# Kernel tuning notes

Measured on AMD Instinct MI355X. Metric: run time of the kernel, lower is better.

## Reference

```python
import jax, jax.numpy as jnp
import numpy as np

NTOKEN = 150000   # len(ui2idx)
NINP   = 64       # opt.d_word_vec
NHID   = 2 * NINP # gnn1 output dim
NEDGE  = 2400000  # hetero static graph edges
B, L   = 64, 200  # batch_size, max_len


def setup_inputs() -> dict:
    key = jax.random.key(0)
    ks = jax.random.split(key, 8)
    def xavier(k, shape):
        scale = (2.0 / (shape[0] + shape[1])) ** 0.5
        return scale * jax.random.normal(k, shape, jnp.float32)
    emb = xavier(ks[0], (NTOKEN, NINP)).at[0].set(0.0)  # padding_idx=0
    W1 = xavier(ks[1], (NINP, NHID))
    b1 = jnp.zeros((NHID,), jnp.float32)
    W2 = xavier(ks[2], (NHID, NINP))
    b2 = jnp.zeros((NINP,), jnp.float32)
    edge_index = jax.random.randint(ks[3], (2, NEDGE), 0, NTOKEN, dtype=jnp.int32).astype(jnp.int64)
    inp = jax.random.randint(ks[4], (B, L), 0, NTOKEN, dtype=jnp.int32).astype(jnp.int64)
    input_timestamp = jax.random.randint(ks[5], (B, L), 0, 300000, dtype=jnp.int32).astype(jnp.int64)
    return {"emb": emb, "W1": W1, "b1": b1, "W2": W2, "b2": b2,
            "input": inp, "input_timestamp": input_timestamp, "edge_index": edge_index}


def gcn_conv(x, W, b, src, dst, n):
    # torch_geometric GCNConv: out = D^{-1/2}(A+I)D^{-1/2} (x W) + b
    h = x @ W                                   # [n, out]
    deg = jnp.zeros((n,), h.dtype).at[dst].add(1.0) + 1.0  # +1 self-loop
    dinv = jax.lax.rsqrt(deg)
    norm = dinv[src] * dinv[dst]                # [E]
    agg = jax.ops.segment_sum(h[src] * norm[:, None], dst, num_segments=n)
    return agg + h * (dinv * dinv)[:, None] + b  # self-loop term + bias


def reference(emb, W1, b1, W2, b2, input, input_timestamp, edge_index):
    src, dst = edge_index[0], edge_index[1]
    h = gcn_conv(emb, W1, b1, src, dst, NTOKEN)      # dropout is identity in eval
    nodes = gcn_conv(h, W2, b2, src, dst, NTOKEN)    # [NTOKEN, NINP]
    # one-hot scatter + einsum 'bt,td->bd' == direct gather
    b_, l_ = input.shape
    return nodes[input.reshape(-1)].reshape(b_, l_, NINP)
```

## Files before the change

### kernel.cpp

```cpp
#include <hip/hip_runtime.h>
#include <hip/hip_bf16.h>

#define NTOKEN 150000
#define NINP   64
#define NEDGE  2400000
#define NPOS   (64*200)

#define NPB    256
#define NBUCK  586
#define EPB    8192
#define NBLK   293
#define CAP    6144

#define O_Z1       0
#define O_HIST     0
#define O_XBF      4800000
#define O_CTOT     9600000
#define O_BSTART   9600640
#define O_DINV     9601280
#define O_ROWSTART 9751296
#define O_BUCK     9901312
#define O_M        12301312
#define O_CVEC     12305408

__device__ __forceinline__ unsigned f2bf(float f) {
    unsigned u = __float_as_uint(f);
    return (u + 0x7FFFu + ((u >> 16) & 1u)) >> 16;
}

__global__ void kX(const float4* __restrict__ X4, uint4* __restrict__ Xbf) {
    int i = blockIdx.x * 256 + threadIdx.x;
    if (i >= NTOKEN * 64 / 8) return;
    float4 a = X4[2 * i], b = X4[2 * i + 1];
    uint4 o;
    o.x = f2bf(a.x) | (f2bf(a.y) << 16);
    o.y = f2bf(a.z) | (f2bf(a.w) << 16);
    o.z = f2bf(b.x) | (f2bf(b.y) << 16);
    o.w = f2bf(b.z) | (f2bf(b.w) << 16);
    Xbf[i] = o;
}

__global__ void kA_hist(const int4* __restrict__ dst4, int* __restrict__ histG) {
    __shared__ int h[NBUCK];
    int tid = threadIdx.x;
    for (int i = tid; i < NBUCK; i += 1024) h[i] = 0;
    __syncthreads();
    int base4 = blockIdx.x * (EPB / 4);
    #pragma unroll
    for (int i = 0; i < EPB / 4096; i++) {
        int idx = base4 + i * 1024 + tid;
        if (idx < NEDGE / 4) {
            int4 d = dst4[idx];
            atomicAdd(&h[d.x >> 8], 1);
            atomicAdd(&h[d.y >> 8], 1);
            atomicAdd(&h[d.z >> 8], 1);
            atomicAdd(&h[d.w >> 8], 1);
        }
    }
    __syncthreads();
    for (int i = tid; i < NBUCK; i += 1024) histG[blockIdx.x * NBUCK + i] = h[i];
}

__global__ void kB1_colscan(int* __restrict__ histG, int* __restrict__ colTotal) {
    __shared__ int sd[256];
    int t = threadIdx.x, b = blockIdx.x;
    int i0 = 2 * t, i1 = 2 * t + 1;
    int v0 = (i0 < NBLK) ? histG[i0 * NBUCK + b] : 0;
    int v1 = (i1 < NBLK) ? histG[i1 * NBUCK + b] : 0;
    int tsum = v0 + v1;
    sd[t] = tsum;
    __syncthreads();
    for (int off = 1; off < 256; off <<= 1) {
        int x = (t >= off) ? sd[t - off] : 0;
        __syncthreads();
        sd[t] += x;
        __syncthreads();
    }
    int excl = sd[t] - tsum;
    if (i0 < NBLK) histG[i0 * NBUCK + b] = excl;
    if (i1 < NBLK) histG[i1 * NBUCK + b] = excl + v0;
    if (t == 255) colTotal[b] = sd[255];
}

__global__ void kB2s(const int* __restrict__ colTotal, int* __restrict__ bucketStart,
                     const float* __restrict__ W1, const float* __restrict__ b1,
                     const float* __restrict__ W2,
                     float* __restrict__ M, float* __restrict__ cvec) {
    int bb = blockIdx.x;
    int t = threadIdx.x;
    if (bb == 0) {
        __shared__ int sd[256];
        int i0 = t * 3, i1 = t * 3 + 1, i2 = t * 3 + 2;
        int v0 = (i0 < NBUCK) ? colTotal[i0] : 0;
        int v1 = (i1 < NBUCK) ? colTotal[i1] : 0;
        int v2 = (i2 < NBUCK) ? colTotal[i2] : 0;
        int tsum = v0 + v1 + v2;
        sd[t] = tsum;
        __syncthreads();
        for (int off = 1; off < 256; off <<= 1) {
            int x = (t >= off) ? sd[t - off] : 0;
            __syncthreads();
            sd[t] += x;
            __syncthreads();
        }
        int excl = sd[t] - tsum;
        if (i0 < NBUCK) bucketStart[i0] = excl;
        if (i1 < NBUCK) bucketStart[i1] = excl + v0;
        if (i2 < NBUCK) bucketStart[i2] = excl + v0 + v1;
        if (t == 255) bucketStart[NBUCK] = NEDGE;
    } else if (bb <= 16) {
        int o = (bb - 1) * 256 + t;
        int i = o >> 6, j = o & 63;
        float s = 0.f;
        #pragma unroll 4
        for (int k = 0; k < 128; k++) s = fmaf(W1[i * 128 + k], W2[k * 64 + j], s);
        M[o] = s;
    } else if (t < 64) {
        float s = 0.f;
        #pragma unroll 4
        for (int k = 0; k < 128; k++) s = fmaf(b1[k], W2[k * 64 + t], s);
        cvec[t] = s;
    }
}

__global__ void kC_scatter(const int4* __restrict__ src4, const int4* __restrict__ dst4,
                           const int* __restrict__ histG, const int* __restrict__ bucketStart,
                           int* __restrict__ bucketPacked) {
    __shared__ int cur[NBUCK];
    int tid = threadIdx.x;
    for (int i = tid; i < NBUCK; i += 1024)
        cur[i] = histG[blockIdx.x * NBUCK + i] + bucketStart[i];
    __syncthreads();
    int base4 = blockIdx.x * (EPB / 4);
    #pragma unroll
    for (int i = 0; i < EPB / 4096; i++) {
        int idx = base4 + i * 1024 + tid;
        if (idx < NEDGE / 4) {
            int4 s = src4[idx];
            int4 d = dst4[idx];
            int p0 = atomicAdd(&cur[d.x >> 8], 1);
            bucketPacked[p0] = (s.x << 8) | (d.x & 255);
            int p1 = atomicAdd(&cur[d.y >> 8], 1);
            bucketPacked[p1] = (s.y << 8) | (d.y & 255);
            int p2 = atomicAdd(&cur[d.z >> 8], 1);
            bucketPacked[p2] = (s.z << 8) | (d.z & 255);
            int p3 = atomicAdd(&cur[d.w >> 8], 1);
            bucketPacked[p3] = (s.w << 8) | (d.w & 255);
        }
    }
}

__global__ void kDE(const int* __restrict__ bucketStart,
                    int* __restrict__ bucketPacked ,
                    float* __restrict__ dinv, int* __restrict__ rowStart) {
    __shared__ int raw[CAP];
    __shared__ int srt[CAP];
    __shared__ int cnt[NPB];
    __shared__ int sd[NPB];
    int t = threadIdx.x, b = blockIdx.x;
    int e0 = bucketStart[b], e1 = bucketStart[b + 1];
    int nE = e1 - e0;
    int nEc = (nE < CAP) ? nE : CAP;
    if (t < NPB) cnt[t] = 0;
    __syncthreads();
    for (int i = t; i < nEc; i += 1024) {
        int p = bucketPacked[e0 + i];
        raw[i] = p;
        atomicAdd(&cnt[p & 255], 1);
    }
    __syncthreads();
    int c = 0;
    if (t < NPB) { c = cnt[t]; sd[t] = c; }
    __syncthreads();
    for (int off = 1; off < 256; off <<= 1) {
        int x = 0;
        if (t < NPB && t >= off) x = sd[t - off];
        __syncthreads();
        if (t < NPB) sd[t] += x;
        __syncthreads();
    }
    if (t < NPB) {
        int excl = sd[t] - c;
        cnt[t] = excl;
        int node = b * NPB + t;
        if (node < NTOKEN) {
            dinv[node] = rsqrtf((float)c + 1.0f);
            rowStart[node] = e0 + excl;
        }
        if (b == NBUCK - 1 && t == 0) rowStart[NTOKEN] = NEDGE;
    }
    __syncthreads();
    for (int i = t; i < nEc; i += 1024) {
        int p = raw[i];
        int pos = atomicAdd(&cnt[p & 255], 1);
        if (pos < CAP) srt[pos] = p >> 8;
    }
    __syncthreads();
    for (int i = t; i < nEc; i += 1024) bucketPacked[e0 + i] = srt[i];
}

__global__ void k_agg(const uint2* __restrict__ Xb, const float* __restrict__ dinv,
                      const int* __restrict__ rowStart, const int* __restrict__ sortedSrc,
                      uint2* __restrict__ Z1b) {
    int g = threadIdx.x >> 4;
    int fl = threadIdx.x & 15;
    int v = blockIdx.x * 16 + g;
    int e0 = rowStart[v], e1 = rowStart[v + 1];
    float dv = dinv[v];
    uint2 xsw = Xb[(size_t)v * 16 + fl];
    float a0x=0.f,a0y=0.f,a0z=0.f,a0w=0.f, a1x=0.f,a1y=0.f,a1z=0.f,a1w=0.f;
    float a2x=0.f,a2y=0.f,a2z=0.f,a2w=0.f, a3x=0.f,a3y=0.f,a3z=0.f,a3w=0.f;
    for (int e = e0; e < e1; e += 8) {
        int m1=e+1<e1, m2=e+2<e1, m3=e+3<e1, m4=e+4<e1, m5=e+5<e1, m6=e+6<e1, m7=e+7<e1;
        int u0 = sortedSrc[e];
        int u1 = sortedSrc[m1 ? e+1 : e];
        int u2 = sortedSrc[m2 ? e+2 : e];
        int u3 = sortedSrc[m3 ? e+3 : e];
        int u4 = sortedSrc[m4 ? e+4 : e];
        int u5 = sortedSrc[m5 ? e+5 : e];
        int u6 = sortedSrc[m6 ? e+6 : e];
        int u7 = sortedSrc[m7 ? e+7 : e];
        float d0 = dinv[u0];
        float d1 = m1 ? dinv[u1] : 0.f;
        float d2 = m2 ? dinv[u2] : 0.f;
        float d3 = m3 ? dinv[u3] : 0.f;
        float d4 = m4 ? dinv[u4] : 0.f;
        float d5 = m5 ? dinv[u5] : 0.f;
        float d6 = m6 ? dinv[u6] : 0.f;
        float d7 = m7 ? dinv[u7] : 0.f;
        uint2 w0 = Xb[(size_t)u0 * 16 + fl];
        uint2 w1 = Xb[(size_t)u1 * 16 + fl];
        uint2 w2 = Xb[(size_t)u2 * 16 + fl];
        uint2 w3 = Xb[(size_t)u3 * 16 + fl];
        uint2 w4 = Xb[(size_t)u4 * 16 + fl];
        uint2 w5 = Xb[(size_t)u5 * 16 + fl];
        uint2 w6 = Xb[(size_t)u6 * 16 + fl];
        uint2 w7 = Xb[(size_t)u7 * 16 + fl];
        #define ACC(d,w,AX,AY,AZ,AW) \
            AX = fmaf(d, __uint_as_float((w).x << 16), AX); \
            AY = fmaf(d, __uint_as_float((w).x & 0xFFFF0000u), AY); \
            AZ = fmaf(d, __uint_as_float((w).y << 16), AZ); \
            AW = fmaf(d, __uint_as_float((w).y & 0xFFFF0000u), AW);
        ACC(d0,w0,a0x,a0y,a0z,a0w)
        ACC(d1,w1,a1x,a1y,a1z,a1w)
        ACC(d2,w2,a2x,a2y,a2z,a2w)
        ACC(d3,w3,a3x,a3y,a3z,a3w)
        ACC(d4,w4,a0x,a0y,a0z,a0w)
        ACC(d5,w5,a1x,a1y,a1z,a1w)
        ACC(d6,w6,a2x,a2y,a2z,a2w)
        ACC(d7,w7,a3x,a3y,a3z,a3w)
        #undef ACC
    }
    float ax = (a0x + a1x) + (a2x + a3x);
    float ay = (a0y + a1y) + (a2y + a3y);
    float az = (a0z + a1z) + (a2z + a3z);
    float aw = (a0w + a1w) + (a2w + a3w);
    float c = dv * dv;
    float ox = c * fmaf(dv, __uint_as_float(xsw.x << 16),        ax);
    float oy = c * fmaf(dv, __uint_as_float(xsw.x & 0xFFFF0000u), ay);
    float oz = c * fmaf(dv, __uint_as_float(xsw.y << 16),        az);
    float ow = c * fmaf(dv, __uint_as_float(xsw.y & 0xFFFF0000u), aw);
    uint2 o;
    o.x = f2bf(ox) | (f2bf(oy) << 16);
    o.y = f2bf(oz) | (f2bf(ow) << 16);
    Z1b[(size_t)v * 16 + fl] = o;
}

__global__ void k_out(const int* __restrict__ inp, const uint2* __restrict__ Z1b,
                      const float* __restrict__ dinv, const int* __restrict__ rowStart,
                      const int* __restrict__ sortedSrc, const float* __restrict__ M,
                      const float* __restrict__ cvec, const float* __restrict__ b2,
                      float* __restrict__ out) {
    int wid = threadIdx.x >> 6;
    int lane = threadIdx.x & 63;
    int g = lane >> 4, fl = lane & 15;
    int p = blockIdx.x * 4 + wid;
    if (p >= NPOS) return;
    int v = inp[p];
    int e0 = rowStart[v], e1 = rowStart[v + 1];
    float ax0=0.f,ay0=0.f,az0=0.f,aw0=0.f,ss0=0.f;
    float ax1=0.f,ay1=0.f,az1=0.f,aw1=0.f,ss1=0.f;
    int e = e0 + g;
    for (; e + 4 < e1; e += 8) {
        int u0 = sortedSrc[e];
        int u1 = sortedSrc[e + 4];
        ss0 += dinv[u0]; ss1 += dinv[u1];
        uint2 z0 = Z1b[(size_t)u0 * 16 + fl];
        uint2 z1 = Z1b[(size_t)u1 * 16 + fl];
        ax0 += __uint_as_float(z0.x << 16);
        ay0 += __uint_as_float(z0.x & 0xFFFF0000u);
        az0 += __uint_as_float(z0.y << 16);
        aw0 += __uint_as_float(z0.y & 0xFFFF0000u);
        ax1 += __uint_as_float(z1.x << 16);
        ay1 += __uint_as_float(z1.x & 0xFFFF0000u);
        az1 += __uint_as_float(z1.y << 16);
        aw1 += __uint_as_float(z1.y & 0xFFFF0000u);
    }
    if (e < e1) {
        int u = sortedSrc[e];
        ss0 += dinv[u];
        uint2 z = Z1b[(size_t)u * 16 + fl];
        ax0 += __uint_as_float(z.x << 16);
        ay0 += __uint_as_float(z.x & 0xFFFF0000u);
        az0 += __uint_as_float(z.y << 16);
        aw0 += __uint_as_float(z.y & 0xFFFF0000u);
    }
    float ax = ax0 + ax1, ay = ay0 + ay1, az = az0 + az1, aw = aw0 + aw1, ss = ss0 + ss1;
    ax += __shfl_xor(ax, 16, 64); ay += __shfl_xor(ay, 16, 64);
    az += __shfl_xor(az, 16, 64); aw += __shfl_xor(aw, 16, 64);
    ss += __shfl_xor(ss, 16, 64);
    ax += __shfl_xor(ax, 32, 64); ay += __shfl_xor(ay, 32, 64);
    az += __shfl_xor(az, 32, 64); aw += __shfl_xor(aw, 32, 64);
    ss += __shfl_xor(ss, 32, 64);
    float dv = dinv[v];
    uint2 zs = Z1b[(size_t)v * 16 + fl];
    float z2x = dv * (ax + __uint_as_float(zs.x << 16));
    float z2y = dv * (ay + __uint_as_float(zs.x & 0xFFFF0000u));
    float z2z = dv * (az + __uint_as_float(zs.y << 16));
    float z2w = dv * (aw + __uint_as_float(zs.y & 0xFFFF0000u));
    float s = dv * (ss + dv);
    float o = fmaf(s, cvec[lane], b2[lane]);
    #pragma unroll
    for (int kb = 0; kb < 16; kb++) {
        float a0 = __shfl(z2x, kb, 64);
        float a1 = __shfl(z2y, kb, 64);
        float a2 = __shfl(z2z, kb, 64);
        float a3 = __shfl(z2w, kb, 64);
        o = fmaf(a0, M[(kb * 4 + 0) * 64 + lane], o);
        o = fmaf(a1, M[(kb * 4 + 1) * 64 + lane], o);
        o = fmaf(a2, M[(kb * 4 + 2) * 64 + lane], o);
        o = fmaf(a3, M[(kb * 4 + 3) * 64 + lane], o);
    }
    out[(size_t)p * 64 + lane] = o;
}

extern "C" void kernel_launch(void* const* d_in, const int* in_sizes, int n_in,
                              void* d_out, int out_size, void* d_ws, size_t ws_size,
                              hipStream_t stream) {
    const float* emb = (const float*)d_in[0];
    const float* W1  = (const float*)d_in[1];
    const float* b1  = (const float*)d_in[2];
    const float* W2  = (const float*)d_in[3];
    const float* b2  = (const float*)d_in[4];
    const int*   inp = (const int*)d_in[5];
    const int*   ei  = (const int*)d_in[7];
    const int* srcArr = ei;
    const int* dstArr = ei + NEDGE;
    float* out = (float*)d_out;

    float* ws         = (float*)d_ws;
    uint2* Z1b        = (uint2*)(ws + O_Z1);
    int*   histG      = (int*)ws + O_HIST;
    uint2* Xbf        = (uint2*)(ws + O_XBF);
    int*   colTotal   = (int*)ws + O_CTOT;
    int*   bucketStart= (int*)ws + O_BSTART;
    float* dinv       = ws + O_DINV;
    int*   rowStart   = (int*)ws + O_ROWSTART;
    int*   buckPacked = (int*)ws + O_BUCK;
    float* M          = ws + O_M;
    float* cvec       = ws + O_CVEC;

    kX         <<<(NTOKEN*64/8 + 255)/256, 256, 0, stream>>>((const float4*)emb, (uint4*)Xbf);
    kA_hist    <<<NBLK,  1024, 0, stream>>>((const int4*)dstArr, histG);
    kB1_colscan<<<NBUCK, 256,  0, stream>>>(histG, colTotal);
    kB2s       <<<18,    256,  0, stream>>>(colTotal, bucketStart, W1, b1, W2, M, cvec);
    kC_scatter <<<NBLK,  1024, 0, stream>>>((const int4*)srcArr, (const int4*)dstArr,
                                            histG, bucketStart, buckPacked);
    kDE        <<<NBUCK, 1024, 0, stream>>>(bucketStart, buckPacked, dinv, rowStart);
    k_agg      <<<NTOKEN/16, 256, 0, stream>>>(Xbf, dinv, rowStart, buckPacked, Z1b);
    k_out      <<<NPOS/4, 256, 0, stream>>>(inp, Z1b, dinv, rowStart,
                                            buckPacked, M, cvec, b2, out);
}
```

Measured before the change: 133.2 us.

## Fuse preprocessing kernels and merge bucket sort into per-bucket aggregation

Merges the bf16 conversion, destination histogram and W1·W2 product into one launch, and folds the bucket-start scan into the scatter kernel, which every block recomputes redundantly. The per-bucket counting sort now happens inside the first-layer aggregation kernel, which reads source indices from shared memory instead of global memory. The goal is fewer launches and one less global round trip of the edge array. In exchange, aggregation uses fewer, larger blocks (586 blocks of 512 threads, each thread group walking 8 nodes serially), which may reduce parallelism. Buckets larger than the smaller shared-memory capacity of 4608 edges would be silently truncated.

```diff
diff --git a/kernel.cpp b/kernel.cpp
--- a/kernel.cpp
+++ b/kernel.cpp
@@ -10,106 +10,66 @@
 #define NBUCK  586
 #define EPB    8192
 #define NBLK   293
-#define CAP    6144
-
-#define O_Z1       0
-#define O_HIST     0
-#define O_XBF      4800000
-#define O_CTOT     9600000
-#define O_BSTART   9600640
-#define O_DINV     9601280
-#define O_ROWSTART 9751296
-#define O_BUCK     9901312
-#define O_M        12301312
-#define O_CVEC     12305408
+#define CAP    4608
+
+#define NXB    1172
+
+#define O_XBF      0
+#define O_Z1       4800000
+#define O_HIST     4800000
+#define O_BUCK     9600000
+#define O_CTOT     12000000
+#define O_BST      12000640
+#define O_DINV     12001280
+#define O_RS       12151296
+#define O_RE       12301312
+#define O_M        12451328
+#define O_CVEC     12455424
 
 __device__ __forceinline__ unsigned f2bf(float f) {
     unsigned u = __float_as_uint(f);
     return (u + 0x7FFFu + ((u >> 16) & 1u)) >> 16;
 }
 
-__global__ void kX(const float4* __restrict__ X4, uint4* __restrict__ Xbf) {
-    int i = blockIdx.x * 256 + threadIdx.x;
-    if (i >= NTOKEN * 64 / 8) return;
-    float4 a = X4[2 * i], b = X4[2 * i + 1];
-    uint4 o;
-    o.x = f2bf(a.x) | (f2bf(a.y) << 16);
-    o.y = f2bf(a.z) | (f2bf(a.w) << 16);
-    o.z = f2bf(b.x) | (f2bf(b.y) << 16);
-    o.w = f2bf(b.z) | (f2bf(b.w) << 16);
-    Xbf[i] = o;
-}
-
-__global__ void kA_hist(const int4* __restrict__ dst4, int* __restrict__ histG) {
+__global__ void __launch_bounds__(1024) k1(
+        const float4* __restrict__ X4, uint4* __restrict__ Xbf,
+        const int4* __restrict__ dst4, int* __restrict__ histG,
+        const float* __restrict__ W1, const float* __restrict__ b1,
+        const float* __restrict__ W2, float* __restrict__ M,
+        float* __restrict__ cvec) {
     __shared__ int h[NBUCK];
-    int tid = threadIdx.x;
-    for (int i = tid; i < NBUCK; i += 1024) h[i] = 0;
-    __syncthreads();
-    int base4 = blockIdx.x * (EPB / 4);
-    #pragma unroll
-    for (int i = 0; i < EPB / 4096; i++) {
-        int idx = base4 + i * 1024 + tid;
-        if (idx < NEDGE / 4) {
-            int4 d = dst4[idx];
-            atomicAdd(&h[d.x >> 8], 1);
-            atomicAdd(&h[d.y >> 8], 1);
-            atomicAdd(&h[d.z >> 8], 1);
-            atomicAdd(&h[d.w >> 8], 1);
-        }
-    }
-    __syncthreads();
-    for (int i = tid; i < NBUCK; i += 1024) histG[blockIdx.x * NBUCK + i] = h[i];
-}
-
-__global__ void kB1_colscan(int* __restrict__ histG, int* __restrict__ colTotal) {
-    __shared__ int sd[256];
-    int t = threadIdx.x, b = blockIdx.x;
-    int i0 = 2 * t, i1 = 2 * t + 1;
-    int v0 = (i0 < NBLK) ? histG[i0 * NBUCK + b] : 0;
-    int v1 = (i1 < NBLK) ? histG[i1 * NBUCK + b] : 0;
-    int tsum = v0 + v1;
-    sd[t] = tsum;
-    __syncthreads();
-    for (int off = 1; off < 256; off <<= 1) {
-        int x = (t >= off) ? sd[t - off] : 0;
-        __syncthreads();
-        sd[t] += x;
-        __syncthreads();
-    }
-    int excl = sd[t] - tsum;
-    if (i0 < NBLK) histG[i0 * NBUCK + b] = excl;
-    if (i1 < NBLK) histG[i1 * NBUCK + b] = excl + v0;
-    if (t == 255) colTotal[b] = sd[255];
-}
-
-__global__ void kB2s(const int* __restrict__ colTotal, int* __restrict__ bucketStart,
-                     const float* __restrict__ W1, const float* __restrict__ b1,
-                     const float* __restrict__ W2,
-                     float* __restrict__ M, float* __restrict__ cvec) {
-    int bb = blockIdx.x;
-    int t = threadIdx.x;
-    if (bb == 0) {
-        __shared__ int sd[256];
-        int i0 = t * 3, i1 = t * 3 + 1, i2 = t * 3 + 2;
-        int v0 = (i0 < NBUCK) ? colTotal[i0] : 0;
-        int v1 = (i1 < NBUCK) ? colTotal[i1] : 0;
-        int v2 = (i2 < NBUCK) ? colTotal[i2] : 0;
-        int tsum = v0 + v1 + v2;
-        sd[t] = tsum;
-        __syncthreads();
-        for (int off = 1; off < 256; off <<= 1) {
-            int x = (t >= off) ? sd[t - off] : 0;
-            __syncthreads();
-            sd[t] += x;
-            __syncthreads();
-        }
-        int excl = sd[t] - tsum;
-        if (i0 < NBUCK) bucketStart[i0] = excl;
-        if (i1 < NBUCK) bucketStart[i1] = excl + v0;
-        if (i2 < NBUCK) bucketStart[i2] = excl + v0 + v1;
-        if (t == 255) bucketStart[NBUCK] = NEDGE;
-    } else if (bb <= 16) {
-        int o = (bb - 1) * 256 + t;
+    int t = threadIdx.x, B = blockIdx.x;
+    if (B < NXB) {
+        int i = B * 1024 + t;
+        if (i < NTOKEN * 64 / 8) {
+            float4 a = X4[2 * i], b = X4[2 * i + 1];
+            uint4 o;
+            o.x = f2bf(a.x) | (f2bf(a.y) << 16);
+            o.y = f2bf(a.z) | (f2bf(a.w) << 16);
+            o.z = f2bf(b.x) | (f2bf(b.y) << 16);
+            o.w = f2bf(b.z) | (f2bf(b.w) << 16);
+            Xbf[i] = o;
+        }
+    } else if (B < NXB + NBLK) {
+        int hb = B - NXB;
+        for (int i = t; i < NBUCK; i += 1024) h[i] = 0;
+        __syncthreads();
+        int base4 = hb * (EPB / 4);
+        #pragma unroll
+        for (int it = 0; it < EPB / 4096; it++) {
+            int idx = base4 + it * 1024 + t;
+            if (idx < NEDGE / 4) {
+                int4 d = dst4[idx];
+                atomicAdd(&h[d.x >> 8], 1);
+                atomicAdd(&h[d.y >> 8], 1);
+                atomicAdd(&h[d.z >> 8], 1);
+                atomicAdd(&h[d.w >> 8], 1);
+            }
+        }
+        __syncthreads();
+        for (int i = t; i < NBUCK; i += 1024) histG[hb * NBUCK + i] = h[i];
+    } else if (B < NXB + NBLK + 4) {
+        int o = (B - NXB - NBLK) * 1024 + t;
         int i = o >> 6, j = o & 63;
         float s = 0.f;
         #pragma unroll 4
@@ -123,18 +83,55 @@
     }
 }
 
-__global__ void kC_scatter(const int4* __restrict__ src4, const int4* __restrict__ dst4,
-                           const int* __restrict__ histG, const int* __restrict__ bucketStart,
-                           int* __restrict__ bucketPacked) {
+__global__ void kB1_colscan(int* __restrict__ histG, int* __restrict__ colTotal) {
+    __shared__ int sd[256];
+    int t = threadIdx.x, b = blockIdx.x;
+    int i0 = 2 * t, i1 = 2 * t + 1;
+    int v0 = (i0 < NBLK) ? histG[i0 * NBUCK + b] : 0;
+    int v1 = (i1 < NBLK) ? histG[i1 * NBUCK + b] : 0;
+    int tsum = v0 + v1;
+    sd[t] = tsum;
+    __syncthreads();
+    for (int off = 1; off < 256; off <<= 1) {
+        int x = (t >= off) ? sd[t - off] : 0;
+        __syncthreads();
+        sd[t] += x;
+        __syncthreads();
+    }
+    int excl = sd[t] - tsum;
+    if (i0 < NBLK) histG[i0 * NBUCK + b] = excl;
+    if (i1 < NBLK) histG[i1 * NBUCK + b] = excl + v0;
+    if (t == 255) colTotal[b] = sd[255];
+}
+
+__global__ void __launch_bounds__(1024) kC_scatter(
+        const int4* __restrict__ src4, const int4* __restrict__ dst4,
+        const int* __restrict__ histG, const int* __restrict__ colTotal,
+        int* __restrict__ bsG, int* __restrict__ bucketPacked) {
+    __shared__ int sd[1024];
+    __shared__ int bs[NBUCK + 1];
     __shared__ int cur[NBUCK];
-    int tid = threadIdx.x;
-    for (int i = tid; i < NBUCK; i += 1024)
-        cur[i] = histG[blockIdx.x * NBUCK + i] + bucketStart[i];
-    __syncthreads();
-    int base4 = blockIdx.x * (EPB / 4);
+    int t = threadIdx.x, B = blockIdx.x;
+    int v0 = (t < NBUCK) ? colTotal[t] : 0;
+    sd[t] = v0;
+    __syncthreads();
+    for (int off = 1; off < 1024; off <<= 1) {
+        int x = (t >= off) ? sd[t - off] : 0;
+        __syncthreads();
+        sd[t] += x;
+        __syncthreads();
+    }
+    if (t < NBUCK) bs[t] = sd[t] - v0;
+    if (t == 0) bs[NBUCK] = NEDGE;
+    __syncthreads();
+    if (B == 0)
+        for (int i = t; i < NBUCK + 1; i += 1024) bsG[i] = bs[i];
+    for (int i = t; i < NBUCK; i += 1024) cur[i] = histG[B * NBUCK + i] + bs[i];
+    __syncthreads();
+    int base4 = B * (EPB / 4);
     #pragma unroll
-    for (int i = 0; i < EPB / 4096; i++) {
-        int idx = base4 + i * 1024 + tid;
+    for (int it = 0; it < EPB / 4096; it++) {
+        int idx = base4 + it * 1024 + t;
         if (idx < NEDGE / 4) {
             int4 s = src4[idx];
             int4 d = dst4[idx];
@@ -150,24 +147,16 @@
     }
 }
 
-__global__ void kDE(const int* __restrict__ bucketStart,
-                    int* __restrict__ bucketPacked ,
-                    float* __restrict__ dinv, int* __restrict__ rowStart) {
-    __shared__ int raw[CAP];
-    __shared__ int srt[CAP];
+__global__ void kDp(const int* __restrict__ bsG, const int* __restrict__ packed,
+                    float* __restrict__ dinv, int* __restrict__ rowStart,
+                    int* __restrict__ rowEnd) {
     __shared__ int cnt[NPB];
     __shared__ int sd[NPB];
     int t = threadIdx.x, b = blockIdx.x;
-    int e0 = bucketStart[b], e1 = bucketStart[b + 1];
-    int nE = e1 - e0;
-    int nEc = (nE < CAP) ? nE : CAP;
+    int e0 = bsG[b], e1 = bsG[b + 1], nE = e1 - e0;
     if (t < NPB) cnt[t] = 0;
     __syncthreads();
-    for (int i = t; i < nEc; i += 1024) {
-        int p = bucketPacked[e0 + i];
-        raw[i] = p;
-        atomicAdd(&cnt[p & 255], 1);
-    }
+    for (int i = t; i < nE; i += 512) atomicAdd(&cnt[packed[e0 + i] & 255], 1);
     __syncthreads();
     int c = 0;
     if (t < NPB) { c = cnt[t]; sd[t] = c; }
@@ -181,103 +170,113 @@
     }
     if (t < NPB) {
         int excl = sd[t] - c;
-        cnt[t] = excl;
         int node = b * NPB + t;
         if (node < NTOKEN) {
             dinv[node] = rsqrtf((float)c + 1.0f);
             rowStart[node] = e0 + excl;
-        }
-        if (b == NBUCK - 1 && t == 0) rowStart[NTOKEN] = NEDGE;
-    }
-    __syncthreads();
-    for (int i = t; i < nEc; i += 1024) {
-        int p = raw[i];
-        int pos = atomicAdd(&cnt[p & 255], 1);
+            rowEnd[node]   = e0 + excl + c;
+        }
+    }
+}
+
+__global__ void __launch_bounds__(512) k_agg(
+        const uint2* __restrict__ Xb, const float* __restrict__ dinv,
+        const int* __restrict__ bsG, const int* __restrict__ rowStart,
+        const int* __restrict__ rowEnd,
+        int* __restrict__ packed ,
+        uint2* __restrict__ Z1b) {
+    __shared__ int srt[CAP];
+    __shared__ int cur[NPB];
+    int t = threadIdx.x, b = blockIdx.x;
+    int e0 = bsG[b], e1 = bsG[b + 1], nE = e1 - e0;
+    int node = b * NPB + t;
+    if (t < NPB) cur[t] = (node < NTOKEN) ? (rowStart[node] - e0) : nE;
+    __syncthreads();
+    for (int i = t; i < nE; i += 512) {
+        int p = packed[e0 + i];
+        int pos = atomicAdd(&cur[p & 255], 1);
         if (pos < CAP) srt[pos] = p >> 8;
     }
     __syncthreads();
-    for (int i = t; i < nEc; i += 1024) bucketPacked[e0 + i] = srt[i];
-}
-
-__global__ void k_agg(const uint2* __restrict__ Xb, const float* __restrict__ dinv,
-                      const int* __restrict__ rowStart, const int* __restrict__ sortedSrc,
-                      uint2* __restrict__ Z1b) {
-    int g = threadIdx.x >> 4;
-    int fl = threadIdx.x & 15;
-    int v = blockIdx.x * 16 + g;
-    int e0 = rowStart[v], e1 = rowStart[v + 1];
-    float dv = dinv[v];
-    uint2 xsw = Xb[(size_t)v * 16 + fl];
-    float a0x=0.f,a0y=0.f,a0z=0.f,a0w=0.f, a1x=0.f,a1y=0.f,a1z=0.f,a1w=0.f;
-    float a2x=0.f,a2y=0.f,a2z=0.f,a2w=0.f, a3x=0.f,a3y=0.f,a3z=0.f,a3w=0.f;
-    for (int e = e0; e < e1; e += 8) {
-        int m1=e+1<e1, m2=e+2<e1, m3=e+3<e1, m4=e+4<e1, m5=e+5<e1, m6=e+6<e1, m7=e+7<e1;
-        int u0 = sortedSrc[e];
-        int u1 = sortedSrc[m1 ? e+1 : e];
-        int u2 = sortedSrc[m2 ? e+2 : e];
-        int u3 = sortedSrc[m3 ? e+3 : e];
-        int u4 = sortedSrc[m4 ? e+4 : e];
-        int u5 = sortedSrc[m5 ? e+5 : e];
-        int u6 = sortedSrc[m6 ? e+6 : e];
-        int u7 = sortedSrc[m7 ? e+7 : e];
-        float d0 = dinv[u0];
-        float d1 = m1 ? dinv[u1] : 0.f;
-        float d2 = m2 ? dinv[u2] : 0.f;
-        float d3 = m3 ? dinv[u3] : 0.f;
-        float d4 = m4 ? dinv[u4] : 0.f;
-        float d5 = m5 ? dinv[u5] : 0.f;
-        float d6 = m6 ? dinv[u6] : 0.f;
-        float d7 = m7 ? dinv[u7] : 0.f;
-        uint2 w0 = Xb[(size_t)u0 * 16 + fl];
-        uint2 w1 = Xb[(size_t)u1 * 16 + fl];
-        uint2 w2 = Xb[(size_t)u2 * 16 + fl];
-        uint2 w3 = Xb[(size_t)u3 * 16 + fl];
-        uint2 w4 = Xb[(size_t)u4 * 16 + fl];
-        uint2 w5 = Xb[(size_t)u5 * 16 + fl];
-        uint2 w6 = Xb[(size_t)u6 * 16 + fl];
-        uint2 w7 = Xb[(size_t)u7 * 16 + fl];
-        #define ACC(d,w,AX,AY,AZ,AW) \
-            AX = fmaf(d, __uint_as_float((w).x << 16), AX); \
-            AY = fmaf(d, __uint_as_float((w).x & 0xFFFF0000u), AY); \
-            AZ = fmaf(d, __uint_as_float((w).y << 16), AZ); \
-            AW = fmaf(d, __uint_as_float((w).y & 0xFFFF0000u), AW);
-        ACC(d0,w0,a0x,a0y,a0z,a0w)
-        ACC(d1,w1,a1x,a1y,a1z,a1w)
-        ACC(d2,w2,a2x,a2y,a2z,a2w)
-        ACC(d3,w3,a3x,a3y,a3z,a3w)
-        ACC(d4,w4,a0x,a0y,a0z,a0w)
-        ACC(d5,w5,a1x,a1y,a1z,a1w)
-        ACC(d6,w6,a2x,a2y,a2z,a2w)
-        ACC(d7,w7,a3x,a3y,a3z,a3w)
-        #undef ACC
-    }
-    float ax = (a0x + a1x) + (a2x + a3x);
-    float ay = (a0y + a1y) + (a2y + a3y);
-    float az = (a0z + a1z) + (a2z + a3z);
-    float aw = (a0w + a1w) + (a2w + a3w);
-    float c = dv * dv;
-    float ox = c * fmaf(dv, __uint_as_float(xsw.x << 16),        ax);
-    float oy = c * fmaf(dv, __uint_as_float(xsw.x & 0xFFFF0000u), ay);
-    float oz = c * fmaf(dv, __uint_as_float(xsw.y << 16),        az);
-    float ow = c * fmaf(dv, __uint_as_float(xsw.y & 0xFFFF0000u), aw);
-    uint2 o;
-    o.x = f2bf(ox) | (f2bf(oy) << 16);
-    o.y = f2bf(oz) | (f2bf(ow) << 16);
-    Z1b[(size_t)v * 16 + fl] = o;
+    for (int i = t; i < nE; i += 512) packed[e0 + i] = srt[i];
+    int g = t >> 4, fl = t & 15;
+    for (int j = 0; j < 8; j++) {
+        int v = b * NPB + g * 8 + j;
+        if (v >= NTOKEN) break;
+        int ls = rowStart[v] - e0, le = rowEnd[v] - e0;
+        float dv = dinv[v];
+        uint2 xsw = Xb[(size_t)v * 16 + fl];
+        float a0x=0.f,a0y=0.f,a0z=0.f,a0w=0.f, a1x=0.f,a1y=0.f,a1z=0.f,a1w=0.f;
+        float a2x=0.f,a2y=0.f,a2z=0.f,a2w=0.f, a3x=0.f,a3y=0.f,a3z=0.f,a3w=0.f;
+        for (int e = ls; e < le; e += 8) {
+            int m1=e+1<le, m2=e+2<le, m3=e+3<le, m4=e+4<le, m5=e+5<le, m6=e+6<le, m7=e+7<le;
+            int u0 = srt[e];
+            int u1 = srt[m1 ? e+1 : e];
+            int u2 = srt[m2 ? e+2 : e];
+            int u3 = srt[m3 ? e+3 : e];
+            int u4 = srt[m4 ? e+4 : e];
+            int u5 = srt[m5 ? e+5 : e];
+            int u6 = srt[m6 ? e+6 : e];
+            int u7 = srt[m7 ? e+7 : e];
+            float d0 = dinv[u0];
+            float d1 = m1 ? dinv[u1] : 0.f;
+            float d2 = m2 ? dinv[u2] : 0.f;
+            float d3 = m3 ? dinv[u3] : 0.f;
+            float d4 = m4 ? dinv[u4] : 0.f;
+            float d5 = m5 ? dinv[u5] : 0.f;
+            float d6 = m6 ? dinv[u6] : 0.f;
+            float d7 = m7 ? dinv[u7] : 0.f;
+            uint2 w0 = Xb[(size_t)u0 * 16 + fl];
+            uint2 w1 = Xb[(size_t)u1 * 16 + fl];
+            uint2 w2 = Xb[(size_t)u2 * 16 + fl];
+            uint2 w3 = Xb[(size_t)u3 * 16 + fl];
+            uint2 w4 = Xb[(size_t)u4 * 16 + fl];
+            uint2 w5 = Xb[(size_t)u5 * 16 + fl];
+            uint2 w6 = Xb[(size_t)u6 * 16 + fl];
+            uint2 w7 = Xb[(size_t)u7 * 16 + fl];
+            #define ACC(d,w,AX,AY,AZ,AW) \
+                AX = fmaf(d, __uint_as_float((w).x << 16), AX); \
+                AY = fmaf(d, __uint_as_float((w).x & 0xFFFF0000u), AY); \
+                AZ = fmaf(d, __uint_as_float((w).y << 16), AZ); \
+                AW = fmaf(d, __uint_as_float((w).y & 0xFFFF0000u), AW);
+            ACC(d0,w0,a0x,a0y,a0z,a0w)
+            ACC(d1,w1,a1x,a1y,a1z,a1w)
+            ACC(d2,w2,a2x,a2y,a2z,a2w)
+            ACC(d3,w3,a3x,a3y,a3z,a3w)
+            ACC(d4,w4,a0x,a0y,a0z,a0w)
+            ACC(d5,w5,a1x,a1y,a1z,a1w)
+            ACC(d6,w6,a2x,a2y,a2z,a2w)
+            ACC(d7,w7,a3x,a3y,a3z,a3w)
+            #undef ACC
+        }
+        float ax = (a0x + a1x) + (a2x + a3x);
+        float ay = (a0y + a1y) + (a2y + a3y);
+        float az = (a0z + a1z) + (a2z + a3z);
+        float aw = (a0w + a1w) + (a2w + a3w);
+        float c = dv * dv;
+        float ox = c * fmaf(dv, __uint_as_float(xsw.x << 16),         ax);
+        float oy = c * fmaf(dv, __uint_as_float(xsw.x & 0xFFFF0000u), ay);
+        float oz = c * fmaf(dv, __uint_as_float(xsw.y << 16),         az);
+        float ow = c * fmaf(dv, __uint_as_float(xsw.y & 0xFFFF0000u), aw);
+        uint2 o;
+        o.x = f2bf(ox) | (f2bf(oy) << 16);
+        o.y = f2bf(oz) | (f2bf(ow) << 16);
+        Z1b[(size_t)v * 16 + fl] = o;
+    }
 }
 
 __global__ void k_out(const int* __restrict__ inp, const uint2* __restrict__ Z1b,
                       const float* __restrict__ dinv, const int* __restrict__ rowStart,
-                      const int* __restrict__ sortedSrc, const float* __restrict__ M,
-                      const float* __restrict__ cvec, const float* __restrict__ b2,
-                      float* __restrict__ out) {
+                      const int* __restrict__ rowEnd, const int* __restrict__ sortedSrc,
+                      const float* __restrict__ M, const float* __restrict__ cvec,
+                      const float* __restrict__ b2, float* __restrict__ out) {
     int wid = threadIdx.x >> 6;
     int lane = threadIdx.x & 63;
     int g = lane >> 4, fl = lane & 15;
     int p = blockIdx.x * 4 + wid;
     if (p >= NPOS) return;
     int v = inp[p];
-    int e0 = rowStart[v], e1 = rowStart[v + 1];
+    int e0 = rowStart[v], e1 = rowEnd[v];
     float ax0=0.f,ay0=0.f,az0=0.f,aw0=0.f,ss0=0.f;
     float ax1=0.f,ay1=0.f,az1=0.f,aw1=0.f,ss1=0.f;
     int e = e0 + g;
@@ -349,25 +348,27 @@
     float* out = (float*)d_out;
 
     float* ws         = (float*)d_ws;
+    uint2* Xbf        = (uint2*)(ws + O_XBF);
     uint2* Z1b        = (uint2*)(ws + O_Z1);
     int*   histG      = (int*)ws + O_HIST;
-    uint2* Xbf        = (uint2*)(ws + O_XBF);
+    int*   buckPacked = (int*)ws + O_BUCK;
     int*   colTotal   = (int*)ws + O_CTOT;
-    int*   bucketStart= (int*)ws + O_BSTART;
+    int*   bsG        = (int*)ws + O_BST;
     float* dinv       = ws + O_DINV;
-    int*   rowStart   = (int*)ws + O_ROWSTART;
-    int*   buckPacked = (int*)ws + O_BUCK;
+    int*   rowStart   = (int*)ws + O_RS;
+    int*   rowEnd     = (int*)ws + O_RE;
     float* M          = ws + O_M;
     float* cvec       = ws + O_CVEC;
 
-    kX         <<<(NTOKEN*64/8 + 255)/256, 256, 0, stream>>>((const float4*)emb, (uint4*)Xbf);
-    kA_hist    <<<NBLK,  1024, 0, stream>>>((const int4*)dstArr, histG);
+    k1         <<<NXB + NBLK + 5, 1024, 0, stream>>>((const float4*)emb, (uint4*)Xbf,
+                                                     (const int4*)dstArr, histG,
+                                                     W1, b1, W2, M, cvec);
     kB1_colscan<<<NBUCK, 256,  0, stream>>>(histG, colTotal);
-    kB2s       <<<18,    256,  0, stream>>>(colTotal, bucketStart, W1, b1, W2, M, cvec);
     kC_scatter <<<NBLK,  1024, 0, stream>>>((const int4*)srcArr, (const int4*)dstArr,
-                                            histG, bucketStart, buckPacked);
-    kDE        <<<NBUCK, 1024, 0, stream>>>(bucketStart, buckPacked, dinv, rowStart);
-    k_agg      <<<NTOKEN/16, 256, 0, stream>>>(Xbf, dinv, rowStart, buckPacked, Z1b);
-    k_out      <<<NPOS/4, 256, 0, stream>>>(inp, Z1b, dinv, rowStart,
+                                            histG, colTotal, bsG, buckPacked);
+    kDp        <<<NBUCK, 512,  0, stream>>>(bsG, buckPacked, dinv, rowStart, rowEnd);
+    k_agg      <<<NBUCK, 512,  0, stream>>>(Xbf, dinv, bsG, rowStart, rowEnd,
+                                            buckPacked, Z1b);
+    k_out      <<<NPOS/4, 256, 0, stream>>>(inp, Z1b, dinv, rowStart, rowEnd,
                                             buckPacked, M, cvec, b2, out);
 }
```

Measured after the change: 137.0 us. 1.03x slower.
